# Performance work log

Hardware: AMD Instinct MI355X
Metric: run time of the kernel (lower is better)

## Reference

```python
import jax, jax.numpy as jnp
import numpy as np

N, E, DIM, HEADS = 50000, 600000, 128, 4
C = DIM // HEADS  # per-head channels = 32
NEG_SLOPE = 0.2
LN_EPS = 1e-5


def setup_inputs() -> dict:
    key = jax.random.key(0)
    ks = jax.random.split(key, 6)
    x = jax.random.normal(ks[0], (N, DIM), dtype=jnp.float32)
    edge_index = jax.random.randint(ks[1], (2, E), 0, N, dtype=jnp.int32)
    W = jax.random.normal(ks[2], (DIM, DIM), dtype=jnp.float32) / np.sqrt(DIM).astype(np.float32)
    b = jnp.zeros((DIM,), jnp.float32)
    att_src = jax.random.normal(ks[3], (HEADS, C), dtype=jnp.float32) * 0.1
    att_dst = jax.random.normal(ks[4], (HEADS, C), dtype=jnp.float32) * 0.1
    gamma = jnp.ones((DIM,), jnp.float32)
    beta = jnp.zeros((DIM,), jnp.float32)
    return {"x": x, "W": W, "b": b, "att_src": att_src, "att_dst": att_dst,
            "gamma": gamma, "beta": beta, "edge_index": edge_index}


def _gat_conv(x, W, b, att_src, att_dst, src, dst):
    # linear projection, per-head view: [N, H, C]
    h = (x @ W).reshape(N, HEADS, C)
    # per-node attention logits: [N, H]
    a_s = jnp.einsum('nhc,hc->nh', h, att_src)
    a_d = jnp.einsum('nhc,hc->nh', h, att_dst)
    # per-edge logits with leaky relu: [Etot, H]
    e = jax.nn.leaky_relu(a_s[src] + a_d[dst], negative_slope=NEG_SLOPE)
    # segment softmax over incoming edges of each dst node
    m = jax.ops.segment_max(e, dst, num_segments=N)
    ez = jnp.exp(e - m[dst])
    denom = jax.ops.segment_sum(ez, dst, num_segments=N) + 1e-16
    alpha = ez / denom[dst]  # [Etot, H]
    # weighted scatter-aggregation: [N, H, C]
    out = jax.ops.segment_sum(alpha[:, :, None] * h[src], dst, num_segments=N)
    return out.reshape(N, DIM) + b


def reference(x, W, b, att_src, att_dst, gamma, beta, edge_index):
    # add self loops (PyG GATConv default add_self_loops=True)
    loops = jnp.arange(N, dtype=edge_index.dtype)
    src = jnp.concatenate([edge_index[0], loops])
    dst = jnp.concatenate([edge_index[1], loops])
    g = _gat_conv(x, W, b, att_src, att_dst, src, dst)
    # residual + GELU (torch exact erf GELU) + LayerNorm; dropout = identity (eval)
    y = x + jax.nn.gelu(g, approximate=False)
    mu = jnp.mean(y, axis=-1, keepdims=True)
    var = jnp.mean(jnp.square(y - mu), axis=-1, keepdims=True)
    return (y - mu) / jnp.sqrt(var + LN_EPS) * gamma + beta
```

## Files before the change

kernel.cpp:

```cpp
#include <hip/hip_runtime.h>
#include <math.h>

#define DIMC 128
#define HEADSC 4

typedef __attribute__((ext_vector_type(8))) short bf16x8;
typedef __attribute__((ext_vector_type(4))) float f32x4;
typedef __attribute__((ext_vector_type(2))) float f32x2;

static __device__ __forceinline__ short f2bf(float f) {
    unsigned u = __builtin_bit_cast(unsigned, f);
    unsigned r = (u + 0x7fff + ((u >> 16) & 1)) >> 16;
    return (short)r;
}
static __device__ __forceinline__ float blo(unsigned q) {
    return __builtin_bit_cast(float, q << 16);
}
static __device__ __forceinline__ float bhi(unsigned q) {
    return __builtin_bit_cast(float, q & 0xffff0000u);
}

__global__ __launch_bounds__(256) void gemm_hist_kernel(
    const float* __restrict__ x, const float* __restrict__ W,
    const float* __restrict__ att_src, const float* __restrict__ att_dst,
    const int* __restrict__ dst, int E,
    unsigned short* __restrict__ hb, float* __restrict__ a_s, float* __restrict__ a_d,
    int* __restrict__ counts, int N, int nstrip)
{
    const int lane = threadIdx.x & 63;
    const int wv   = threadIdx.x >> 6;
    const int pr   = wv >> 1;
    const int half = wv & 1;
    const int l15  = lane & 15;
    const int lg   = lane >> 4;

    bf16x8 bfr[4][4];
#pragma unroll
    for (int ct = 0; ct < 4; ++ct) {
#pragma unroll
        for (int kk = 0; kk < 4; ++kk) {
            const float* wp = W + (size_t)(kk * 32 + lg * 8) * DIMC + half * 64 + ct * 16 + l15;
#pragma unroll
            for (int jj = 0; jj < 8; ++jj)
                bfr[ct][kk][jj] = f2bf(wp[(size_t)jj * DIMC]);
        }
    }
    float attS[4], attD[4];
#pragma unroll
    for (int ct = 0; ct < 4; ++ct) {
        attS[ct] = att_src[half * 64 + ct * 16 + l15];
        attD[ct] = att_dst[half * 64 + ct * 16 + l15];
    }

    for (int s = blockIdx.x * 2 + pr; s < nstrip; s += gridDim.x * 2) {
        const int row = s * 16 + l15;
        const float* xp = x + (size_t)row * DIMC + lg * 8;
        bf16x8 afr[4];
#pragma unroll
        for (int kk = 0; kk < 4; ++kk) {
            f32x4 v0 = *(const f32x4*)(xp + kk * 32);
            f32x4 v1 = *(const f32x4*)(xp + kk * 32 + 4);
#pragma unroll
            for (int jj = 0; jj < 4; ++jj) {
                afr[kk][jj]     = f2bf(v0[jj]);
                afr[kk][jj + 4] = f2bf(v1[jj]);
            }
        }
        f32x4 acc[4] = {};
#pragma unroll
        for (int ct = 0; ct < 4; ++ct) {
#pragma unroll
            for (int kk = 0; kk < 4; ++kk)
                acc[ct] = __builtin_amdgcn_mfma_f32_16x16x32_bf16(
                    afr[kk], bfr[ct][kk], acc[ct], 0, 0, 0);
        }
        unsigned short* hp = hb + (size_t)(s * 16) * DIMC + half * 64;
#pragma unroll
        for (int ct = 0; ct < 4; ++ct)
#pragma unroll
            for (int reg = 0; reg < 4; ++reg)
                hp[(size_t)(lg * 4 + reg) * DIMC + ct * 16 + l15] =
                    (unsigned short)f2bf(acc[ct][reg]);
#pragma unroll
        for (int reg = 0; reg < 4; ++reg) {
            float s0 = fmaf(acc[0][reg], attS[0], acc[1][reg] * attS[1]);
            float s1 = fmaf(acc[2][reg], attS[2], acc[3][reg] * attS[3]);
            float d0 = fmaf(acc[0][reg], attD[0], acc[1][reg] * attD[1]);
            float d1 = fmaf(acc[2][reg], attD[2], acc[3][reg] * attD[3]);
#pragma unroll
            for (int mk = 1; mk < 16; mk <<= 1) {
                s0 += __shfl_xor(s0, mk);
                s1 += __shfl_xor(s1, mk);
                d0 += __shfl_xor(d0, mk);
                d1 += __shfl_xor(d1, mk);
            }
            if (l15 == 0) {
                const int r = s * 16 + lg * 4 + reg;
                a_s[r * HEADSC + half * 2 + 0] = s0;
                a_s[r * HEADSC + half * 2 + 1] = s1;
                a_d[r * HEADSC + half * 2 + 0] = d0;
                a_d[r * HEADSC + half * 2 + 1] = d1;
            }
        }
    }

    const int tid = blockIdx.x * 256 + threadIdx.x;
    const int stride = gridDim.x * 256;
    if (((E & 3) == 0) && ((((size_t)dst) & 15) == 0)) {
        const int E4 = E >> 2;
        for (int i = tid; i < E4; i += stride) {
            const int4 d4 = ((const int4*)dst)[i];
            atomicAdd(&counts[d4.x], 1);
            atomicAdd(&counts[d4.y], 1);
            atomicAdd(&counts[d4.z], 1);
            atomicAdd(&counts[d4.w], 1);
        }
    } else {
        for (int i = tid; i < E; i += stride) atomicAdd(&counts[dst[i]], 1);
    }
}

__global__ __launch_bounds__(256) void scan1_kernel(
    const int* __restrict__ counts, int* __restrict__ partial, int N)
{
    const int t = threadIdx.x, i = blockIdx.x * 256 + t;
    int v = (i < N) ? counts[i] + 1 : 0;
    int s = v;
#pragma unroll
    for (int mk = 1; mk < 64; mk <<= 1) s += __shfl_xor(s, mk);
    __shared__ int ws[4];
    if ((t & 63) == 0) ws[t >> 6] = s;
    __syncthreads();
    if (t == 0) partial[blockIdx.x] = ws[0] + ws[1] + ws[2] + ws[3];
}

__global__ __launch_bounds__(256) void scan23_kernel(
    const int* __restrict__ counts, const int* __restrict__ partial,
    int* __restrict__ S, int N, int P)
{
    const int t = threadIdx.x;
    const int lane = t & 63, wv = t >> 6;
    __shared__ int ws[4];
    __shared__ int ex[256];

    int pv = (t < P) ? partial[t] : 0;
    int xs = pv;
#pragma unroll
    for (int d = 1; d < 64; d <<= 1) { int tt = __shfl_up(xs, d); if (lane >= d) xs += tt; }
    if (lane == 63) ws[wv] = xs;
    __syncthreads();
    int wof = 0;
#pragma unroll
    for (int w = 0; w < 4; ++w) wof += (w < wv) ? ws[w] : 0;
    ex[t] = wof + xs - pv;
    __syncthreads();
    const int prefix = ex[blockIdx.x];
    __syncthreads();

    const int i = blockIdx.x * 256 + t;
    int v = (i < N) ? counts[i] + 1 : 0;
    int s2 = v;
#pragma unroll
    for (int d = 1; d < 64; d <<= 1) { int tt = __shfl_up(s2, d); if (lane >= d) s2 += tt; }
    if (lane == 63) ws[wv] = s2;
    __syncthreads();
    int wof2 = 0;
#pragma unroll
    for (int w = 0; w < 4; ++w) wof2 += (w < wv) ? ws[w] : 0;
    if (i < N) S[i] = prefix + wof2 + s2 - v;
}

__global__ void scatter_kernel(const int* __restrict__ ei, int E, int N,
                               int* __restrict__ S, int* __restrict__ rec)
{
    const int tid = blockIdx.x * blockDim.x + threadIdx.x;
    const int stride = gridDim.x * blockDim.x;
    if (((E & 3) == 0) && ((((size_t)ei) & 15) == 0)) {
        const int E4 = E >> 2;
        const int4* s4p = (const int4*)ei;
        const int4* d4p = (const int4*)(ei + E);
        for (int i = tid; i < E4; i += stride) {
            const int4 s4 = s4p[i];
            const int4 d4 = d4p[i];
            rec[atomicAdd(&S[d4.x], 1)] = s4.x;
            rec[atomicAdd(&S[d4.y], 1)] = s4.y;
            rec[atomicAdd(&S[d4.z], 1)] = s4.z;
            rec[atomicAdd(&S[d4.w], 1)] = s4.w;
        }
    } else {
        for (int i = tid; i < E; i += stride)
            rec[atomicAdd(&S[ei[E + i]], 1)] = ei[i];
    }
    for (int n = tid; n < N; n += stride)
        rec[atomicAdd(&S[n], 1)] = n;
}

__global__ __launch_bounds__(256) void node_kernel(
    const float* __restrict__ x, const unsigned short* __restrict__ hb,
    const int* __restrict__ S, const int* __restrict__ rec,
    const float* __restrict__ a_s, const float* __restrict__ a_d,
    const float* __restrict__ bias, const float* __restrict__ gamma,
    const float* __restrict__ beta, float* __restrict__ out, int N)
{
    const int wv = threadIdx.x >> 6;
    const int lane = threadIdx.x & 63;
    const int c2 = lane * 2;
    const int head = lane >> 4;

    for (int n = blockIdx.x * 4 + wv; n < N; n += gridDim.x * 4) {
        const int beg = __builtin_amdgcn_readfirstlane(n ? S[n - 1] : 0);
        const int end = __builtin_amdgcn_readfirstlane(S[n]);
        const float adh = a_d[n * HEADSC + head];
        float den = 0.f, e0 = 0.f, e1 = 0.f, o0 = 0.f, o1 = 0.f;
        int i = beg;
        const int e4 = beg + ((end - beg) & ~3);
        for (; i < e4; i += 4) {
            const int s0 = rec[i + 0], s1 = rec[i + 1];
            const int s2 = rec[i + 2], s3 = rec[i + 3];
            float t0 = a_s[s0 * HEADSC + head] + adh;
            float t1 = a_s[s1 * HEADSC + head] + adh;
            float t2 = a_s[s2 * HEADSC + head] + adh;
            float t3 = a_s[s3 * HEADSC + head] + adh;
            const unsigned q0 = *(const unsigned*)(hb + (size_t)s0 * DIMC + c2);
            const unsigned q1 = *(const unsigned*)(hb + (size_t)s1 * DIMC + c2);
            const unsigned q2 = *(const unsigned*)(hb + (size_t)s2 * DIMC + c2);
            const unsigned q3 = *(const unsigned*)(hb + (size_t)s3 * DIMC + c2);
            t0 = (t0 > 0.f) ? t0 : 0.2f * t0;
            t1 = (t1 > 0.f) ? t1 : 0.2f * t1;
            t2 = (t2 > 0.f) ? t2 : 0.2f * t2;
            t3 = (t3 > 0.f) ? t3 : 0.2f * t3;
            const float p0 = __expf(t0), p1 = __expf(t1);
            const float p2 = __expf(t2), p3 = __expf(t3);
            den += (p0 + p1) + (p2 + p3);
            e0 = fmaf(p0, blo(q0), e0); e1 = fmaf(p0, bhi(q0), e1);
            o0 = fmaf(p1, blo(q1), o0); o1 = fmaf(p1, bhi(q1), o1);
            e0 = fmaf(p2, blo(q2), e0); e1 = fmaf(p2, bhi(q2), e1);
            o0 = fmaf(p3, blo(q3), o0); o1 = fmaf(p3, bhi(q3), o1);
        }
        for (; i < end; ++i) {
            const int s0 = rec[i];
            float t0 = a_s[s0 * HEADSC + head] + adh;
            const unsigned q0 = *(const unsigned*)(hb + (size_t)s0 * DIMC + c2);
            t0 = (t0 > 0.f) ? t0 : 0.2f * t0;
            const float p0 = __expf(t0);
            den += p0;
            e0 = fmaf(p0, blo(q0), e0);
            e1 = fmaf(p0, bhi(q0), e1);
        }
        const float acc0 = e0 + o0, acc1 = e1 + o1;

        const float inv = 1.f / (den + 1e-16f);
        const f32x2 bi = *(const f32x2*)(bias + c2);
        float g0 = acc0 * inv + bi.x;
        float g1 = acc1 * inv + bi.y;
        const float ge0 = 0.5f * g0 * (1.f + erff(g0 * 0.70710678118654752f));
        const float ge1 = 0.5f * g1 * (1.f + erff(g1 * 0.70710678118654752f));
        const f32x2 xv = *(const f32x2*)(x + (size_t)n * DIMC + c2);
        const float y0 = xv.x + ge0;
        const float y1 = xv.y + ge1;
        float s1 = y0 + y1, s2 = y0 * y0 + y1 * y1;
#pragma unroll
        for (int mk = 1; mk < 64; mk <<= 1) {
            s1 += __shfl_xor(s1, mk);
            s2 += __shfl_xor(s2, mk);
        }
        const float mu = s1 * (1.f / DIMC);
        const float var = s2 * (1.f / DIMC) - mu * mu;
        const float rstd = rsqrtf(var + 1e-5f);
        const f32x2 ga = *(const f32x2*)(gamma + c2);
        const f32x2 be = *(const f32x2*)(beta + c2);
        f32x2 o;
        o.x = (y0 - mu) * rstd * ga.x + be.x;
        o.y = (y1 - mu) * rstd * ga.y + be.y;
        *(f32x2*)(out + (size_t)n * DIMC + c2) = o;
    }
}

extern "C" void kernel_launch(void* const* d_in, const int* in_sizes, int n_in,
                              void* d_out, int out_size, void* d_ws, size_t ws_size,
                              hipStream_t stream)
{
    const float* x       = (const float*)d_in[0];
    const float* W       = (const float*)d_in[1];
    const float* bias    = (const float*)d_in[2];
    const float* att_src = (const float*)d_in[3];
    const float* att_dst = (const float*)d_in[4];
    const float* gamma   = (const float*)d_in[5];
    const float* beta    = (const float*)d_in[6];
    const int*   ei      = (const int*)d_in[7];

    const int N = in_sizes[0] / DIMC;
    const int E = in_sizes[7] / 2;

    unsigned short* hb = (unsigned short*)d_ws;
    float* a_s   = (float*)(hb + (size_t)N * DIMC);
    float* a_d   = a_s + (size_t)N * HEADSC;
    int* counts  = (int*)(a_d + (size_t)N * HEADSC);
    int* S       = counts + N;
    int* partial = S + N;
    int* rec     = partial + 256;

    hipMemsetAsync(counts, 0, sizeof(int) * (size_t)N, stream);

    const int nstrip = (N + 15) / 16;
    gemm_hist_kernel<<<784, 256, 0, stream>>>(x, W, att_src, att_dst, ei + E, E,
                                              hb, a_s, a_d, counts, N, nstrip);
    const int nb1 = (N + 255) / 256;
    scan1_kernel<<<nb1, 256, 0, stream>>>(counts, partial, N);
    scan23_kernel<<<nb1, 256, 0, stream>>>(counts, partial, S, N, nb1);
    scatter_kernel<<<640, 256, 0, stream>>>(ei, E, N, S, rec);
    node_kernel<<<(N + 3) / 4, 256, 0, stream>>>(
        x, hb, S, rec, a_s, a_d, bias, gamma, beta, (float*)d_out, N);
}
```

Baseline: 200.2 us.

## Rework GEMM wave split, merge scans into one kernel, widen node gather unroll

Each GEMM block now handles one 16-row strip, with each of its four waves computing one 32-column head, so per-head logits need no cross-pair combine. The GEMM launch bounds add an occupancy hint. The two-kernel scan is replaced by a single 1024-thread block that scans serial chunks per thread, which removes one launch but serialises about 50 elements per thread. The node aggregation loop now issues 8 predicated gathers per iteration instead of 4 plus a tail loop, exposing more memory-level parallelism. Grid sizes change for the GEMM and scatter kernels.

```diff
diff --git a/kernel.cpp b/kernel.cpp
--- a/kernel.cpp
+++ b/kernel.cpp
@@ -20,7 +20,7 @@
     return __builtin_bit_cast(float, q & 0xffff0000u);
 }
 
-__global__ __launch_bounds__(256) void gemm_hist_kernel(
+__global__ __launch_bounds__(256, 2) void gemm_hist_kernel(
     const float* __restrict__ x, const float* __restrict__ W,
     const float* __restrict__ att_src, const float* __restrict__ att_dst,
     const int* __restrict__ dst, int E,
@@ -28,31 +28,29 @@
     int* __restrict__ counts, int N, int nstrip)
 {
     const int lane = threadIdx.x & 63;
-    const int wv   = threadIdx.x >> 6;
-    const int pr   = wv >> 1;
-    const int half = wv & 1;
+    const int q    = threadIdx.x >> 6;
     const int l15  = lane & 15;
     const int lg   = lane >> 4;
 
-    bf16x8 bfr[4][4];
-#pragma unroll
-    for (int ct = 0; ct < 4; ++ct) {
+    bf16x8 bfr[2][4];
+#pragma unroll
+    for (int ct = 0; ct < 2; ++ct) {
 #pragma unroll
         for (int kk = 0; kk < 4; ++kk) {
-            const float* wp = W + (size_t)(kk * 32 + lg * 8) * DIMC + half * 64 + ct * 16 + l15;
+            const float* wp = W + (size_t)(kk * 32 + lg * 8) * DIMC + q * 32 + ct * 16 + l15;
 #pragma unroll
             for (int jj = 0; jj < 8; ++jj)
                 bfr[ct][kk][jj] = f2bf(wp[(size_t)jj * DIMC]);
         }
     }
-    float attS[4], attD[4];
-#pragma unroll
-    for (int ct = 0; ct < 4; ++ct) {
-        attS[ct] = att_src[half * 64 + ct * 16 + l15];
-        attD[ct] = att_dst[half * 64 + ct * 16 + l15];
-    }
-
-    for (int s = blockIdx.x * 2 + pr; s < nstrip; s += gridDim.x * 2) {
+    float attS[2], attD[2];
+#pragma unroll
+    for (int ct = 0; ct < 2; ++ct) {
+        attS[ct] = att_src[q * 32 + ct * 16 + l15];
+        attD[ct] = att_dst[q * 32 + ct * 16 + l15];
+    }
+
+    for (int s = blockIdx.x; s < nstrip; s += gridDim.x) {
         const int row = s * 16 + l15;
         const float* xp = x + (size_t)row * DIMC + lg * 8;
         bf16x8 afr[4];
@@ -66,40 +64,34 @@
                 afr[kk][jj + 4] = f2bf(v1[jj]);
             }
         }
-        f32x4 acc[4] = {};
-#pragma unroll
-        for (int ct = 0; ct < 4; ++ct) {
+        f32x4 acc[2] = {};
+#pragma unroll
+        for (int ct = 0; ct < 2; ++ct) {
 #pragma unroll
             for (int kk = 0; kk < 4; ++kk)
                 acc[ct] = __builtin_amdgcn_mfma_f32_16x16x32_bf16(
                     afr[kk], bfr[ct][kk], acc[ct], 0, 0, 0);
         }
-        unsigned short* hp = hb + (size_t)(s * 16) * DIMC + half * 64;
-#pragma unroll
-        for (int ct = 0; ct < 4; ++ct)
+        unsigned short* hp = hb + (size_t)(s * 16) * DIMC + q * 32;
+#pragma unroll
+        for (int ct = 0; ct < 2; ++ct)
 #pragma unroll
             for (int reg = 0; reg < 4; ++reg)
                 hp[(size_t)(lg * 4 + reg) * DIMC + ct * 16 + l15] =
                     (unsigned short)f2bf(acc[ct][reg]);
 #pragma unroll
         for (int reg = 0; reg < 4; ++reg) {
-            float s0 = fmaf(acc[0][reg], attS[0], acc[1][reg] * attS[1]);
-            float s1 = fmaf(acc[2][reg], attS[2], acc[3][reg] * attS[3]);
-            float d0 = fmaf(acc[0][reg], attD[0], acc[1][reg] * attD[1]);
-            float d1 = fmaf(acc[2][reg], attD[2], acc[3][reg] * attD[3]);
+            float sv = fmaf(acc[0][reg], attS[0], acc[1][reg] * attS[1]);
+            float dv = fmaf(acc[0][reg], attD[0], acc[1][reg] * attD[1]);
 #pragma unroll
             for (int mk = 1; mk < 16; mk <<= 1) {
-                s0 += __shfl_xor(s0, mk);
-                s1 += __shfl_xor(s1, mk);
-                d0 += __shfl_xor(d0, mk);
-                d1 += __shfl_xor(d1, mk);
+                sv += __shfl_xor(sv, mk);
+                dv += __shfl_xor(dv, mk);
             }
             if (l15 == 0) {
                 const int r = s * 16 + lg * 4 + reg;
-                a_s[r * HEADSC + half * 2 + 0] = s0;
-                a_s[r * HEADSC + half * 2 + 1] = s1;
-                a_d[r * HEADSC + half * 2 + 0] = d0;
-                a_d[r * HEADSC + half * 2 + 1] = d1;
+                a_s[r * HEADSC + q] = sv;
+                a_d[r * HEADSC + q] = dv;
             }
         }
     }
@@ -120,54 +112,33 @@
     }
 }
 
-__global__ __launch_bounds__(256) void scan1_kernel(
-    const int* __restrict__ counts, int* __restrict__ partial, int N)
-{
-    const int t = threadIdx.x, i = blockIdx.x * 256 + t;
-    int v = (i < N) ? counts[i] + 1 : 0;
-    int s = v;
-#pragma unroll
-    for (int mk = 1; mk < 64; mk <<= 1) s += __shfl_xor(s, mk);
-    __shared__ int ws[4];
-    if ((t & 63) == 0) ws[t >> 6] = s;
-    __syncthreads();
-    if (t == 0) partial[blockIdx.x] = ws[0] + ws[1] + ws[2] + ws[3];
-}
-
-__global__ __launch_bounds__(256) void scan23_kernel(
-    const int* __restrict__ counts, const int* __restrict__ partial,
-    int* __restrict__ S, int N, int P)
+__global__ __launch_bounds__(1024) void scan_kernel(
+    const int* __restrict__ counts, int* __restrict__ S, int N)
 {
     const int t = threadIdx.x;
+    const int CH = (N + 1023) >> 10;
+    const int lo = t * CH;
+    const int hi = (lo + CH < N) ? lo + CH : N;
+    int sum = 0;
+    for (int i = lo; i < hi; ++i) sum += counts[i] + 1;
+
     const int lane = t & 63, wv = t >> 6;
-    __shared__ int ws[4];
-    __shared__ int ex[256];
-
-    int pv = (t < P) ? partial[t] : 0;
-    int xs = pv;
-#pragma unroll
-    for (int d = 1; d < 64; d <<= 1) { int tt = __shfl_up(xs, d); if (lane >= d) xs += tt; }
+    int xs = sum;
+#pragma unroll
+    for (int d = 1; d < 64; d <<= 1) {
+        int tt = __shfl_up(xs, d);
+        if (lane >= d) xs += tt;
+    }
+    __shared__ int ws[16], wo[16];
     if (lane == 63) ws[wv] = xs;
     __syncthreads();
-    int wof = 0;
-#pragma unroll
-    for (int w = 0; w < 4; ++w) wof += (w < wv) ? ws[w] : 0;
-    ex[t] = wof + xs - pv;
+    if (t == 0) {
+        int s = 0;
+        for (int w = 0; w < 16; ++w) { wo[w] = s; s += ws[w]; }
+    }
     __syncthreads();
-    const int prefix = ex[blockIdx.x];
-    __syncthreads();
-
-    const int i = blockIdx.x * 256 + t;
-    int v = (i < N) ? counts[i] + 1 : 0;
-    int s2 = v;
-#pragma unroll
-    for (int d = 1; d < 64; d <<= 1) { int tt = __shfl_up(s2, d); if (lane >= d) s2 += tt; }
-    if (lane == 63) ws[wv] = s2;
-    __syncthreads();
-    int wof2 = 0;
-#pragma unroll
-    for (int w = 0; w < 4; ++w) wof2 += (w < wv) ? ws[w] : 0;
-    if (i < N) S[i] = prefix + wof2 + s2 - v;
+    int excl = wo[wv] + xs - sum;
+    for (int i = lo; i < hi; ++i) { S[i] = excl; excl += counts[i] + 1; }
 }
 
 __global__ void scatter_kernel(const int* __restrict__ ei, int E, int N,
@@ -211,43 +182,31 @@
         const int beg = __builtin_amdgcn_readfirstlane(n ? S[n - 1] : 0);
         const int end = __builtin_amdgcn_readfirstlane(S[n]);
         const float adh = a_d[n * HEADSC + head];
-        float den = 0.f, e0 = 0.f, e1 = 0.f, o0 = 0.f, o1 = 0.f;
-        int i = beg;
-        const int e4 = beg + ((end - beg) & ~3);
-        for (; i < e4; i += 4) {
-            const int s0 = rec[i + 0], s1 = rec[i + 1];
-            const int s2 = rec[i + 2], s3 = rec[i + 3];
-            float t0 = a_s[s0 * HEADSC + head] + adh;
-            float t1 = a_s[s1 * HEADSC + head] + adh;
-            float t2 = a_s[s2 * HEADSC + head] + adh;
-            float t3 = a_s[s3 * HEADSC + head] + adh;
-            const unsigned q0 = *(const unsigned*)(hb + (size_t)s0 * DIMC + c2);
-            const unsigned q1 = *(const unsigned*)(hb + (size_t)s1 * DIMC + c2);
-            const unsigned q2 = *(const unsigned*)(hb + (size_t)s2 * DIMC + c2);
-            const unsigned q3 = *(const unsigned*)(hb + (size_t)s3 * DIMC + c2);
-            t0 = (t0 > 0.f) ? t0 : 0.2f * t0;
-            t1 = (t1 > 0.f) ? t1 : 0.2f * t1;
-            t2 = (t2 > 0.f) ? t2 : 0.2f * t2;
-            t3 = (t3 > 0.f) ? t3 : 0.2f * t3;
-            const float p0 = __expf(t0), p1 = __expf(t1);
-            const float p2 = __expf(t2), p3 = __expf(t3);
-            den += (p0 + p1) + (p2 + p3);
-            e0 = fmaf(p0, blo(q0), e0); e1 = fmaf(p0, bhi(q0), e1);
-            o0 = fmaf(p1, blo(q1), o0); o1 = fmaf(p1, bhi(q1), o1);
-            e0 = fmaf(p2, blo(q2), e0); e1 = fmaf(p2, bhi(q2), e1);
-            o0 = fmaf(p3, blo(q3), o0); o1 = fmaf(p3, bhi(q3), o1);
-        }
-        for (; i < end; ++i) {
-            const int s0 = rec[i];
-            float t0 = a_s[s0 * HEADSC + head] + adh;
-            const unsigned q0 = *(const unsigned*)(hb + (size_t)s0 * DIMC + c2);
-            t0 = (t0 > 0.f) ? t0 : 0.2f * t0;
-            const float p0 = __expf(t0);
-            den += p0;
-            e0 = fmaf(p0, blo(q0), e0);
-            e1 = fmaf(p0, bhi(q0), e1);
-        }
-        const float acc0 = e0 + o0, acc1 = e1 + o1;
+        float den = 0.f, A0 = 0.f, A1 = 0.f, B0 = 0.f, B1 = 0.f;
+        for (int i = beg; i < end; i += 8) {
+            int ss[8];
+            float tt[8];
+            unsigned qq[8];
+#pragma unroll
+            for (int u = 0; u < 8; ++u)
+                ss[u] = rec[(i + u < end) ? i + u : beg];
+#pragma unroll
+            for (int u = 0; u < 8; ++u)
+                tt[u] = a_s[ss[u] * HEADSC + head] + adh;
+#pragma unroll
+            for (int u = 0; u < 8; ++u)
+                qq[u] = *(const unsigned*)(hb + (size_t)ss[u] * DIMC + c2);
+#pragma unroll
+            for (int u = 0; u < 8; ++u) {
+                float e = tt[u];
+                e = (e > 0.f) ? e : 0.2f * e;
+                float p = (i + u < end) ? __expf(e) : 0.f;
+                den += p;
+                if (u & 1) { B0 = fmaf(p, blo(qq[u]), B0); B1 = fmaf(p, bhi(qq[u]), B1); }
+                else       { A0 = fmaf(p, blo(qq[u]), A0); A1 = fmaf(p, bhi(qq[u]), A1); }
+            }
+        }
+        const float acc0 = A0 + B0, acc1 = A1 + B1;
 
         const float inv = 1.f / (den + 1e-16f);
         const f32x2 bi = *(const f32x2*)(bias + c2);
@@ -297,18 +256,15 @@
     float* a_d   = a_s + (size_t)N * HEADSC;
     int* counts  = (int*)(a_d + (size_t)N * HEADSC);
     int* S       = counts + N;
-    int* partial = S + N;
-    int* rec     = partial + 256;
+    int* rec     = S + N;
 
     hipMemsetAsync(counts, 0, sizeof(int) * (size_t)N, stream);
 
     const int nstrip = (N + 15) / 16;
-    gemm_hist_kernel<<<784, 256, 0, stream>>>(x, W, att_src, att_dst, ei + E, E,
-                                              hb, a_s, a_d, counts, N, nstrip);
-    const int nb1 = (N + 255) / 256;
-    scan1_kernel<<<nb1, 256, 0, stream>>>(counts, partial, N);
-    scan23_kernel<<<nb1, 256, 0, stream>>>(counts, partial, S, N, nb1);
-    scatter_kernel<<<640, 256, 0, stream>>>(ei, E, N, S, rec);
+    gemm_hist_kernel<<<1024, 256, 0, stream>>>(x, W, att_src, att_dst, ei + E, E,
+                                               hb, a_s, a_d, counts, N, nstrip);
+    scan_kernel<<<1, 1024, 0, stream>>>(counts, S, N);
+    scatter_kernel<<<1024, 256, 0, stream>>>(ei, E, N, S, rec);
     node_kernel<<<(N + 3) / 4, 256, 0, stream>>>(
         x, hb, S, rec, a_s, a_d, bias, gamma, beta, (float*)d_out, N);
 }
```

After: 273.1 us. 36.4% more time.
